# Performance work log

Measured on AMD Instinct MI355X. Metric: run time of the kernel, lower is better.

The kernel has to match this reference:

```python
import jax, jax.numpy as jnp
import numpy as np

EPS = 1e-5
NEG = jnp.float32(-1e30)


def _mha(q_in, kv, in_w, in_b, out_w, out_b, n_heads, allowed=None):
    # torch nn.MultiheadAttention (batch_first, eval mode)
    B, Nq, D = q_in.shape
    hd = D // n_heads
    wq, wk, wv = jnp.split(in_w, 3, axis=0)
    bq, bk, bv = jnp.split(in_b, 3)
    q = (q_in @ wq.T + bq).reshape(B, Nq, n_heads, hd).transpose(0, 2, 1, 3)
    k = (kv @ wk.T + bk).reshape(B, -1, n_heads, hd).transpose(0, 2, 1, 3)
    v = (kv @ wv.T + bv).reshape(B, -1, n_heads, hd).transpose(0, 2, 1, 3)
    s = jnp.einsum('bhqd,bhkd->bhqk', q, k) / jnp.sqrt(jnp.float32(hd))
    if allowed is not None:
        s = jnp.where(allowed[:, None, :, :], s, NEG)
    a = jax.nn.softmax(s, axis=-1)
    o = jnp.einsum('bhqk,bhkd->bhqd', a, v).transpose(0, 2, 1, 3).reshape(B, Nq, D)
    o = o @ out_w.T + out_b
    if allowed is not None:
        # rows with no allowed keys: torch would NaN; we zero them (deterministic)
        o = jnp.where(allowed.any(-1)[..., None], o, 0.0)
    return o


def _layernorm(x, g, b):
    mu = x.mean(-1, keepdims=True)
    var = ((x - mu) ** 2).mean(-1, keepdims=True)
    return (x - mu) * jax.lax.rsqrt(var + EPS) * g + b


def setup_inputs() -> dict:
    key = jax.random.key(0)
    B, N, D, NH = 128, 128, 512, 8
    ks = jax.random.split(key, 16)
    s = 0.02
    return {
        'H': jax.random.normal(ks[0], (B, N, D), jnp.float32),
        'pred_heads': jax.random.randint(ks[1], (B, N), 0, N, jnp.int32),
        'mask': jnp.ones((B, N), jnp.int32),
        'head_in_w': jax.random.normal(ks[2], (3 * D, D)) * s,
        'head_in_b': jnp.zeros((3 * D,), jnp.float32),
        'head_out_w': jax.random.normal(ks[3], (D, D)) * s,
        'head_out_b': jnp.zeros((D,), jnp.float32),
        'sib_in_w': jax.random.normal(ks[4], (3 * D, D)) * s,
        'sib_in_b': jnp.zeros((3 * D,), jnp.float32),
        'sib_out_w': jax.random.normal(ks[5], (D, D)) * s,
        'sib_out_b': jnp.zeros((D,), jnp.float32),
        'child_w': jax.random.normal(ks[6], (D, 2 * D)) * s,
        'child_b': jnp.zeros((D,), jnp.float32),
        'gate_w': jax.random.normal(ks[7], (D, 4 * D)) * s,
        'gate_b': jnp.zeros((D,), jnp.float32),
        'trans_w': jax.random.normal(ks[8], (D, 4 * D)) * s,
        'trans_b': jnp.zeros((D,), jnp.float32),
        'ln_g': jnp.ones((D,), jnp.float32),
        'ln_b': jnp.zeros((D,), jnp.float32),
    }


def reference(H, pred_heads, mask, head_in_w, head_in_b, head_out_w, head_out_b,
              sib_in_w, sib_in_b, sib_out_w, sib_out_b, child_w, child_b,
              gate_w, gate_b, trans_w, trans_b, ln_g, ln_b):
    B, N, D = H.shape
    NH = 8
    heads = jnp.clip(pred_heads, 0, N - 1)  # [B,N]
    maskb = mask.astype(bool)

    # 1) head message: gather each node's head repr, attend Q=H, K=V=head_repr
    head_repr = jnp.take_along_axis(H, heads[..., None], axis=1)  # [B,N,D]
    head_msg = _mha(H, head_repr, head_in_w, head_in_b, head_out_w, head_out_b, NH)

    # 2) child aggregation: vectorized scatter-add replacing the Python loop.
    # loop runs d in [1, length) with mask a prefix -> valid = mask & (d >= 1)
    valid = maskb & (jnp.arange(N) >= 1)  # [B,N]
    contrib = H * valid[..., None].astype(H.dtype)
    flat_idx = (jnp.arange(B)[:, None] * N + heads).reshape(-1)
    child_sum = jnp.zeros((B * N, D), H.dtype).at[flat_idx].add(
        contrib.reshape(B * N, D)).reshape(B, N, D)
    child_count = jnp.zeros((B * N,), H.dtype).at[flat_idx].add(
        valid.reshape(-1).astype(H.dtype)).reshape(B, N, 1)
    child_avg = child_sum / jnp.maximum(child_count, 1.0)
    child_msg = jax.nn.gelu(
        jnp.concatenate([H, child_avg], -1) @ child_w.T + child_b,
        approximate=False)

    # 3) sibling attention (N <= 128 branch): same head, not self, both masked-in
    same_head = heads[:, :, None] == heads[:, None, :]
    eye = jnp.eye(N, dtype=bool)[None]
    allowed = same_head & ~eye & maskb[:, None, :] & maskb[:, :, None]
    sib_msg = _mha(H, H, sib_in_w, sib_in_b, sib_out_w, sib_out_b, NH, allowed=allowed)

    # 4) gated fusion + residual + layernorm
    combined = jnp.concatenate([H, head_msg, child_msg, sib_msg], -1)
    gate = jax.nn.sigmoid(combined @ gate_w.T + gate_b)
    update = jax.nn.gelu(combined @ trans_w.T + trans_b, approximate=False)
    return _layernorm(H + gate * update, ln_g, ln_b)
```

## Files before the change

### kernel.cpp

```cpp
#include <hip/hip_runtime.h>
#include <hip/hip_bf16.h>

typedef __bf16 bf16x8 __attribute__((ext_vector_type(8)));
typedef float f32x4 __attribute__((ext_vector_type(4)));

__device__ __forceinline__ void gload16(const void* g, void* l) {
  __builtin_amdgcn_global_load_lds(
      (const __attribute__((address_space(1))) unsigned int*)g,
      (__attribute__((address_space(3))) unsigned int*)l, 16, 0, 0);
}

__device__ __forceinline__ float gelu_f(float x) {
  return 0.5f * x * (1.f + erff(x * 0.70710678118654752f));
}
__device__ __forceinline__ float sigmoid_f(float x) {
  return 1.f / (1.f + __expf(-x));
}

template<int EPI>
__global__ __launch_bounds__(512, 2)
void gemm8_kernel(const __hip_bfloat16* __restrict__ A0, int lda0,
                  const __hip_bfloat16* __restrict__ A1, int lda1,
                  const __hip_bfloat16* __restrict__ A2, int lda2,
                  int ks1, int ks2,
                  const __hip_bfloat16* __restrict__ B, int ldb,
                  const float* __restrict__ bias,
                  const float* __restrict__ fvec,
                  const float* __restrict__ flags,
                  void* __restrict__ C, int ldc, int K)
{
  extern __shared__ __align__(16) char lds[];
  const int t = threadIdx.x;
  const int l = t & 63;
  const int w = t >> 6;
  const int l15 = l & 15, lg = (l >> 4) & 3;
  const int orig = blockIdx.y * gridDim.x + blockIdx.x;
  const int nwg = gridDim.x * gridDim.y;
  const int gy = gridDim.y;
  const int xcd = orig & 7, rk = orig >> 3, q = nwg >> 3, r = nwg & 7;
  const int bid = (xcd < r ? xcd * (q + 1) : r * (q + 1) + (xcd - r) * q) + rk;
  const int m0 = (bid % gy) * 256;
  const int n0 = (bid / gy) * 256;

  const int srow = t >> 2;
  const int kc8 = ((t & 3) ^ ((t >> 3) & 3)) * 8;
  const int mbase = (w >> 2) * 128;
  const int nbase = (w & 3) * 64;
  const int swz = (l15 >> 1) & 3;
  const int kslot = (lg ^ swz) * 8;
  int aoff[8], boff[4];
#pragma unroll
  for (int mf = 0; mf < 8; ++mf) aoff[mf] = (mbase + mf * 16 + l15) * 32 + kslot;
#pragma unroll
  for (int nf = 0; nf < 4; ++nf) boff[nf] = (nbase + nf * 16 + l15) * 32 + kslot;

  auto segA = [&](int k0, const __hip_bfloat16*& Ap, int& ldA, int& krel) {
    if (k0 >= ks2)      { Ap = A2; ldA = lda2; krel = k0 - ks2; }
    else if (k0 >= ks1) { Ap = A1; ldA = lda1; krel = k0 - ks1; }
    else                { Ap = A0; ldA = lda0; krel = k0; }
  };
  auto stageA = [&](int buf, const __hip_bfloat16* Ap, int ldA, int krel) {
    char* base = lds + buf * 32768 + t * 16;
    gload16(Ap + (size_t)(m0 + srow) * ldA + krel + kc8, base);
    gload16(Ap + (size_t)(m0 + 128 + srow) * ldA + krel + kc8, base + 8192);
  };
  auto stageB = [&](int buf, int k0) {
    char* base = lds + buf * 32768 + 16384 + t * 16;
    gload16(B + (size_t)(n0 + srow) * ldb + k0 + kc8, base);
    gload16(B + (size_t)(n0 + 128 + srow) * ldb + k0 + kc8, base + 8192);
  };

  f32x4 acc[8][4] = {};
  const int NT = K >> 5;

#pragma unroll 1
  for (int pt = 0; pt < 3; ++pt) {
    const __hip_bfloat16* Ap; int ldA, krel;
    segA(pt * 32, Ap, ldA, krel);
    stageA(pt, Ap, ldA, krel);
    stageB(pt, pt * 32);
  }
  asm volatile("s_waitcnt vmcnt(8)" ::: "memory");
  __builtin_amdgcn_s_barrier();
  __builtin_amdgcn_sched_barrier(0);

#pragma unroll 1
  for (int tt = 0; tt < NT; ++tt) {
    const int buf = tt & 3;
    const __hip_bfloat16* As = (const __hip_bfloat16*)(lds + buf * 32768);
    const __hip_bfloat16* Bs = (const __hip_bfloat16*)(lds + buf * 32768 + 16384);
    const int pf = tt + 3;
    const bool do_pf = pf < NT;
    const int pbuf = pf & 3;
    const __hip_bfloat16* Ap = A0; int ldA = lda0, krel = 0;
    if (do_pf) segA(pf * 32, Ap, ldA, krel);

    bf16x8 bv[4], av[4];
#pragma unroll
    for (int nf = 0; nf < 4; ++nf) bv[nf] = *(const bf16x8*)(Bs + boff[nf]);
#pragma unroll
    for (int mf = 0; mf < 4; ++mf) av[mf] = *(const bf16x8*)(As + aoff[mf]);
    if (do_pf) stageA(pbuf, Ap, ldA, krel);
    __builtin_amdgcn_s_setprio(1);
#pragma unroll
    for (int mf = 0; mf < 4; ++mf)
#pragma unroll
      for (int nf = 0; nf < 4; ++nf)
        acc[mf][nf] = __builtin_amdgcn_mfma_f32_16x16x32_bf16(av[mf], bv[nf], acc[mf][nf], 0, 0, 0);
    __builtin_amdgcn_s_setprio(0);

#pragma unroll
    for (int mf = 0; mf < 4; ++mf) av[mf] = *(const bf16x8*)(As + aoff[mf + 4]);
    if (do_pf) stageB(pbuf, pf * 32);
    __builtin_amdgcn_s_setprio(1);
#pragma unroll
    for (int mf = 0; mf < 4; ++mf)
#pragma unroll
      for (int nf = 0; nf < 4; ++nf)
        acc[mf + 4][nf] = __builtin_amdgcn_mfma_f32_16x16x32_bf16(av[mf], bv[nf], acc[mf + 4][nf], 0, 0, 0);
    __builtin_amdgcn_s_setprio(0);

    __builtin_amdgcn_sched_barrier(0);
    if (tt + 3 < NT)      asm volatile("s_waitcnt vmcnt(8)" ::: "memory");
    else if (tt + 2 < NT) asm volatile("s_waitcnt vmcnt(4)" ::: "memory");
    else if (tt + 1 < NT) asm volatile("s_waitcnt vmcnt(0)" ::: "memory");
    if (tt + 1 < NT) {
      __builtin_amdgcn_s_barrier();
      __builtin_amdgcn_sched_barrier(0);
    }
  }

  if (EPI == 2) {
#pragma unroll
    for (int mf = 0; mf < 8; ++mf) {
#pragma unroll
      for (int nh = 0; nh < 2; ++nh) {
        const int nf = nh * 2;
        const int sc = n0 + nbase + nf * 16;
        const float bg = bias[sc + l15], bt = bias[sc + 16 + l15];
        const float fg = fvec[sc + l15], ft = fvec[sc + 16 + l15];
        const int ocol = (sc >> 5) * 16 + l15;
#pragma unroll
        for (int j = 0; j < 4; ++j) {
          const int row = m0 + mbase + mf * 16 + lg * 4 + j;
          const float flg = flags[row];
          float g  = acc[mf][nf][j]     + bg + flg * fg;
          float tv = acc[mf][nf + 1][j] + bt + flg * ft;
          ((__hip_bfloat16*)C)[(size_t)row * ldc + ocol] =
              __float2bfloat16(sigmoid_f(g) * gelu_f(tv));
        }
      }
    }
    return;
  }
#pragma unroll
  for (int mf = 0; mf < 8; ++mf)
#pragma unroll
    for (int nf = 0; nf < 4; ++nf) {
      const int col = n0 + nbase + nf * 16 + l15;
      const float bc = bias ? bias[col] : 0.f;
#pragma unroll
      for (int j = 0; j < 4; ++j) {
        const int row = m0 + mbase + mf * 16 + lg * 4 + j;
        ((__hip_bfloat16*)C)[(size_t)row * ldc + col] =
            __float2bfloat16(acc[mf][nf][j] + bc);
      }
    }
}

template<int EPI, bool OBF16>
__global__ __launch_bounds__(256)
void gemm_kernel(const __hip_bfloat16* __restrict__ A0, int lda0,
                 const __hip_bfloat16* __restrict__ A1, int lda1,
                 const __hip_bfloat16* __restrict__ A2, int lda2,
                 int ks1, int ks2,
                 const __hip_bfloat16* __restrict__ B, int ldb,
                 const float* __restrict__ bias,
                 const float* __restrict__ fvec,
                 const float* __restrict__ flags,
                 void* __restrict__ C, int ldc, int K)
{
  __shared__ __align__(16) __hip_bfloat16 As[128 * 32];
  __shared__ __align__(16) __hip_bfloat16 Bs[128 * 32];
  const int t = threadIdx.x;
  const int l = t & 63, w = t >> 6;
  const int gx = gridDim.x;
  int bid = blockIdx.y * gx + blockIdx.x;
  {
    const int nwg = gx * gridDim.y;
    const int xcd = bid & 7, rk = bid >> 3, q = nwg >> 3, r = nwg & 7;
    bid = (xcd < r ? xcd * (q + 1) : r * (q + 1) + (xcd - r) * q) + rk;
  }
  const int m0 = (bid / gx) * 128, n0 = (bid % gx) * 128;
  const int wm = (w >> 1) * 64, wn = (w & 1) * 64;
  const int l15 = l & 15, lg = l >> 4;

  const int r0 = t >> 2;
  const int kk0 = ((t & 3) ^ ((t >> 3) & 3)) * 8;
  char* lA = (char*)As + t * 16;
  char* lB = (char*)Bs + t * 16;
  const size_t boff1 = (size_t)(n0 + r0) * ldb + kk0;
  const size_t boff2 = (size_t)(n0 + r0 + 64) * ldb + kk0;

  int aoffR[4], boffR[4];
#pragma unroll
  for (int i = 0; i < 4; ++i) {
    const int ra = wm + i * 16 + l15;
    aoffR[i] = ra * 32 + ((lg ^ ((ra >> 1) & 3)) * 8);
    const int rb = wn + i * 16 + l15;
    boffR[i] = rb * 32 + ((lg ^ ((rb >> 1) & 3)) * 8);
  }
  f32x4 acc[4][4] = {};

#pragma unroll 1
  for (int seg = 0; seg < 3; ++seg) {
    const __hip_bfloat16* Ap;
    int ldA, kb, ke;
    if (seg == 0)      { Ap = A0; ldA = lda0; kb = 0;   ke = ks1; }
    else if (seg == 1) { Ap = A1; ldA = lda1; kb = ks1; ke = ks2; }
    else               { Ap = A2; ldA = lda2; kb = ks2; ke = K;   }
    if (kb >= ke) continue;
    const size_t aoff1 = (size_t)(m0 + r0) * ldA + kk0;
    const size_t aoff2 = (size_t)(m0 + r0 + 64) * ldA + kk0;
    for (int k0 = kb; k0 < ke; k0 += 32) {
      const int kr = k0 - kb;
      gload16(Ap + aoff1 + kr, lA);
      gload16(Ap + aoff2 + kr, lA + 4096);
      gload16(B + boff1 + k0, lB);
      gload16(B + boff2 + k0, lB + 4096);
      __syncthreads();
      bf16x8 af[4], bfr[4];
#pragma unroll
      for (int i = 0; i < 4; ++i) {
        af[i]  = *(const bf16x8*)((const __hip_bfloat16*)As + aoffR[i]);
        bfr[i] = *(const bf16x8*)((const __hip_bfloat16*)Bs + boffR[i]);
      }
#pragma unroll
      for (int mi = 0; mi < 4; ++mi)
#pragma unroll
        for (int ni = 0; ni < 4; ++ni)
          acc[mi][ni] = __builtin_amdgcn_mfma_f32_16x16x32_bf16(af[mi], bfr[ni], acc[mi][ni], 0, 0, 0);
      __syncthreads();
    }
  }

#pragma unroll
  for (int mi = 0; mi < 4; ++mi)
#pragma unroll
    for (int ni = 0; ni < 4; ++ni) {
      const int col = n0 + wn + ni * 16 + l15;
      const float bc = bias ? bias[col] : 0.f;
#pragma unroll
      for (int j = 0; j < 4; ++j) {
        const int row = m0 + wm + mi * 16 + lg * 4 + j;
        float v = acc[mi][ni][j] + bc;
        if (EPI == 1) v = gelu_f(v);
        if (OBF16) ((__hip_bfloat16*)C)[(size_t)row * ldc + col] = __float2bfloat16(v);
        else       ((float*)C)[(size_t)row * ldc + col] = v;
      }
    }
}

__global__ __launch_bounds__(256)
void attn_kernel(const __hip_bfloat16* __restrict__ QKV,
                 const int* __restrict__ pred_heads,
                 const int* __restrict__ mask,
                 __hip_bfloat16* __restrict__ Oout,
                 float* __restrict__ flags)
{
  __shared__ __align__(16) __hip_bfloat16 smem[128 * 128];
  __shared__ __align__(16) __hip_bfloat16 Vt[64 * 128];
  __shared__ int hs[128];
  __shared__ int mk[128];
  const bool SIB = blockIdx.x >= 1024;
  const int bh = blockIdx.x & 1023;
  const int b = bh >> 3, h = bh & 7;
  const int qofs = SIB ? 1536 : 0;
  __hip_bfloat16* Ob = Oout + (SIB ? 512 : 0);
  const int t = threadIdx.x, l = t & 63, w = t >> 6;
  const int l15 = l & 15, lg = l >> 4;
  __hip_bfloat16* Qs = smem;
  __hip_bfloat16* Ks = smem + 128 * 64;

  if (t < 128) {
    int hh = pred_heads[b * 128 + t];
    hh = hh < 0 ? 0 : (hh > 127 ? 127 : hh);
    hs[t] = hh;
    mk[t] = mask[b * 128 + t];
  }
  __syncthreads();
  const size_t tb = (size_t)b * 128 * 3072;
  const int co = qofs + h * 64;
#pragma unroll
  for (int it = 0; it < 4; ++it) {
    const int idx = it * 256 + t;
    const int row = idx >> 3;
    const int c8 = (idx & 7) * 8;
    const int sl = ((c8 >> 3) ^ (row & 7)) * 8;
    *(uint4*)(Qs + row * 64 + sl) = *(const uint4*)(QKV + tb + (size_t)row * 3072 + co + c8);
    const int krow = SIB ? row : hs[row];
    *(uint4*)(Ks + row * 64 + sl) = *(const uint4*)(QKV + tb + (size_t)krow * 3072 + co + 512 + c8);
    uint4 vv = *(const uint4*)(QKV + tb + (size_t)krow * 3072 + co + 1024 + c8);
    const __hip_bfloat16* vp = (const __hip_bfloat16*)&vv;
#pragma unroll
    for (int u = 0; u < 8; ++u) {
      const int d = c8 + u;
      Vt[d * 128 + (((row >> 3) ^ (d & 7)) * 8) + (row & 7)] = vp[u];
    }
  }
  __syncthreads();

  const int r0 = w * 32;
  f32x4 s[2][8] = {};
  const int x7 = l15 & 7;
#pragma unroll
  for (int ks = 0; ks < 2; ++ks) {
    const int sl = ((ks * 4 + lg) ^ x7) * 8;
    bf16x8 qa0 = *(const bf16x8*)(Qs + (r0 + l15) * 64 + sl);
    bf16x8 qa1 = *(const bf16x8*)(Qs + (r0 + 16 + l15) * 64 + sl);
#pragma unroll
    for (int nj = 0; nj < 8; ++nj) {
      bf16x8 kb = *(const bf16x8*)(Ks + (nj * 16 + l15) * 64 + sl);
      s[0][nj] = __builtin_amdgcn_mfma_f32_16x16x32_bf16(qa0, kb, s[0][nj], 0, 0, 0);
      s[1][nj] = __builtin_amdgcn_mfma_f32_16x16x32_bf16(qa1, kb, s[1][nj], 0, 0, 0);
    }
  }
  const float scale = 0.125f;
  float inv_sum[2][4];
#pragma unroll
  for (int mi = 0; mi < 2; ++mi) {
#pragma unroll
    for (int j = 0; j < 4; ++j) {
      const int row = r0 + mi * 16 + lg * 4 + j;
      float mx = -1e30f;
#pragma unroll
      for (int nj = 0; nj < 8; ++nj) {
        float v = s[mi][nj][j] * scale;
        bool ok = true;
        if (SIB) {
          int c = nj * 16 + l15;
          ok = (hs[row] == hs[c]) && (row != c) && mk[row] && mk[c];
        }
        mx = fmaxf(mx, ok ? v : -1e30f);
      }
#pragma unroll
      for (int m = 1; m < 16; m <<= 1) mx = fmaxf(mx, __shfl_xor(mx, m));
      float sum = 0.f;
#pragma unroll
      for (int nj = 0; nj < 8; ++nj) {
        float v = s[mi][nj][j] * scale;
        bool ok = true;
        if (SIB) {
          int c = nj * 16 + l15;
          ok = (hs[row] == hs[c]) && (row != c) && mk[row] && mk[c];
        }
        float p = ok ? __expf(v - mx) : 0.f;
        s[mi][nj][j] = p;
        sum += p;
      }
#pragma unroll
      for (int m = 1; m < 16; m <<= 1) sum += __shfl_xor(sum, m);
      inv_sum[mi][j] = sum > 0.f ? 1.f / sum : 0.f;
    }
  }
  __syncthreads();
#pragma unroll
  for (int mi = 0; mi < 2; ++mi)
#pragma unroll
    for (int nj = 0; nj < 8; ++nj)
#pragma unroll
      for (int j = 0; j < 4; ++j) {
        const int rr = r0 + mi * 16 + lg * 4 + j;
        const int cc = nj * 16 + l15;
        smem[rr * 128 + (((cc >> 3) ^ (rr & 7)) * 8) + (cc & 7)] = __float2bfloat16(s[mi][nj][j]);
      }
  __syncthreads();

  f32x4 o[2][4] = {};
#pragma unroll
  for (int js = 0; js < 4; ++js) {
    const int slot = js * 4 + lg;
    const int slp = (slot ^ x7) * 8;
    bf16x8 pa0 = *(const bf16x8*)(smem + (r0 + l15) * 128 + slp);
    bf16x8 pa1 = *(const bf16x8*)(smem + (r0 + 16 + l15) * 128 + slp);
#pragma unroll
    for (int dj = 0; dj < 4; ++dj) {
      bf16x8 vb = *(const bf16x8*)(Vt + (dj * 16 + l15) * 128 + slp);
      o[0][dj] = __builtin_amdgcn_mfma_f32_16x16x32_bf16(pa0, vb, o[0][dj], 0, 0, 0);
      o[1][dj] = __builtin_amdgcn_mfma_f32_16x16x32_bf16(pa1, vb, o[1][dj], 0, 0, 0);
    }
  }
  const int hb = h * 64;
#pragma unroll
  for (int mi = 0; mi < 2; ++mi)
#pragma unroll
    for (int dj = 0; dj < 4; ++dj)
#pragma unroll
      for (int j = 0; j < 4; ++j) {
        const int row = r0 + mi * 16 + lg * 4 + j;
        const int dc = dj * 16 + l15;
        const float val = o[mi][dj][j] * inv_sum[mi][j];
        Ob[(size_t)(b * 128 + row) * 1024 + hb + dc] = __float2bfloat16(val);
      }
  if (SIB && h == 0 && l15 == 0) {
#pragma unroll
    for (int mi = 0; mi < 2; ++mi)
#pragma unroll
      for (int j = 0; j < 4; ++j) {
        const int row = r0 + mi * 16 + lg * 4 + j;
        flags[b * 128 + row] = inv_sum[mi][j] > 0.f ? 1.f : 0.f;
      }
  }
}

__global__ __launch_bounds__(256)
void child_kernel(const __hip_bfloat16* __restrict__ Hbf,
                  const int* __restrict__ pred_heads,
                  const int* __restrict__ mask,
                  __hip_bfloat16* __restrict__ Cavg)
{
  __shared__ float sum[128 * 64];
  __shared__ int cnt[128];
  __shared__ int hsl[128];
  __shared__ int vld[128];
  const int t = threadIdx.x;
  const int b = blockIdx.y, ch = blockIdx.x;
#pragma unroll
  for (int u = 0; u < 32; ++u) sum[u * 256 + t] = 0.f;
  if (t < 128) {
    int hh = pred_heads[b * 128 + t];
    hh = hh < 0 ? 0 : (hh > 127 ? 127 : hh);
    hsl[t] = hh;
    vld[t] = (mask[b * 128 + t] != 0) && (t >= 1);
    cnt[t] = 0;
  }
  __syncthreads();
  if (t < 128 && vld[t]) atomicAdd(&cnt[hsl[t]], 1);
  __syncthreads();
  const int c = t & 63;
  const int isub = t >> 6;
  for (int ii = 0; ii < 32; ++ii) {
    int i = ii * 4 + isub;
    if (vld[i])
      atomicAdd(&sum[hsl[i] * 64 + c],
                __bfloat162float(Hbf[((size_t)b * 128 + i) * 512 + ch * 64 + c]));
  }
  __syncthreads();
#pragma unroll
  for (int u = 0; u < 32; ++u) {
    int idx = u * 256 + t;
    int p = idx >> 6, cc = idx & 63;
    float avg = sum[idx] / fmaxf((float)cnt[p], 1.f);
    Cavg[((size_t)b * 128 + p) * 512 + ch * 64 + cc] = __float2bfloat16(avg);
  }
}

__global__ void prep_kernel(const float* __restrict__ hin_w, const float* __restrict__ sin_w,
                            const float* __restrict__ ch_w, const float* __restrict__ H,
                            __hip_bfloat16* __restrict__ Wqkv, __hip_bfloat16* __restrict__ Wch,
                            __hip_bfloat16* __restrict__ Hbf,
                            const float* __restrict__ gw, const float* __restrict__ tw,
                            const float* __restrict__ gb, const float* __restrict__ tb,
                            __hip_bfloat16* __restrict__ Wf, __hip_bfloat16* __restrict__ Whin,
                            __hip_bfloat16* __restrict__ Wsin, float* __restrict__ bias,
                            const float* __restrict__ hout_w, const float* __restrict__ sout_w,
                            __hip_bfloat16* __restrict__ WhoT, __hip_bfloat16* __restrict__ WsoT)
{
  int gid = blockIdx.x * 256 + threadIdx.x;
  if (gid < 2621440) {
    const float* s; __hip_bfloat16* d; int i;
    if      (gid <  196608) { s = hin_w; d = Wqkv;          i = gid; }
    else if (gid <  393216) { s = sin_w; d = Wqkv + 786432; i = gid - 196608; }
    else if (gid <  524288) { s = ch_w;  d = Wch;           i = gid - 393216; }
    else                    { s = H;     d = Hbf;           i = gid - 524288; }
    i *= 4;
    float4 v = *(const float4*)(s + i);
    union { __hip_bfloat16 h[4]; uint2 u; } p;
    p.h[0] = __float2bfloat16(v.x); p.h[1] = __float2bfloat16(v.y);
    p.h[2] = __float2bfloat16(v.z); p.h[3] = __float2bfloat16(v.w);
    *(uint2*)(d + i) = p.u;
  } else if (gid < 4718592) {
    int idx = gid - 2621440;
    int s = idx >> 11, c = idx & 2047;
    int q = s >> 5, r = s & 31;
    float v = (r < 16) ? gw[(size_t)(q * 16 + r) * 2048 + c]
                       : tw[(size_t)(q * 16 + r - 16) * 2048 + c];
    __hip_bfloat16 hv = __float2bfloat16(v);
    if      (c <  512) Wf[(size_t)s * 2048 + c] = hv;
    else if (c < 1024) Whin[(size_t)s * 512 + (c - 512)] = hv;
    else if (c < 1536) Wf[(size_t)s * 2048 + (c - 512)] = hv;
    else               Wsin[(size_t)s * 512 + (c - 1536)] = hv;
    if (c == 0) bias[s] = (r < 16) ? gb[q * 16 + r] : tb[q * 16 + r - 16];
  } else {
    int idx = gid - 4718592;
    const float* s = hout_w; __hip_bfloat16* d = WhoT;
    if (idx >= 262144) { s = sout_w; d = WsoT; idx -= 262144; }
    int i = idx >> 9, j = idx & 511;
    d[i * 512 + j] = __float2bfloat16(s[(size_t)j * 512 + i]);
  }
}

__global__ __launch_bounds__(256)
void foldbias_kernel(const __hip_bfloat16* __restrict__ Whin, const __hip_bfloat16* __restrict__ Wsin,
                     const float* __restrict__ hob, const float* __restrict__ sob,
                     float* __restrict__ bias_gt, float* __restrict__ fvec)
{
  const int s = blockIdx.x * 256 + threadIdx.x;
  float a = 0.f, c = 0.f;
  for (int j = 0; j < 512; j += 8) {
    bf16x8 wh = *(const bf16x8*)(Whin + (size_t)s * 512 + j);
    bf16x8 wsv = *(const bf16x8*)(Wsin + (size_t)s * 512 + j);
#pragma unroll
    for (int u = 0; u < 8; ++u) {
      a += (float)wh[u] * hob[j + u];
      c += (float)wsv[u] * sob[j + u];
    }
  }
  bias_gt[s] += a;
  fvec[s] = c;
}

__global__ __launch_bounds__(64)
void ln_kernel(const float* __restrict__ H, const __hip_bfloat16* __restrict__ U,
               const float* __restrict__ g, const float* __restrict__ bta,
               float* __restrict__ out)
{
  const int row = blockIdx.x, l = threadIdx.x;
  const size_t hb = (size_t)row * 512;
  const int c0 = l * 8;
  float4 h0 = *(const float4*)(H + hb + c0);
  float4 h1 = *(const float4*)(H + hb + c0 + 4);
  bf16x8 uv = *(const bf16x8*)(U + hb + c0);
  float x[8];
  x[0] = h0.x + (float)uv[0]; x[1] = h0.y + (float)uv[1];
  x[2] = h0.z + (float)uv[2]; x[3] = h0.w + (float)uv[3];
  x[4] = h1.x + (float)uv[4]; x[5] = h1.y + (float)uv[5];
  x[6] = h1.z + (float)uv[6]; x[7] = h1.w + (float)uv[7];
  float sum = 0.f;
#pragma unroll
  for (int u = 0; u < 8; ++u) sum += x[u];
#pragma unroll
  for (int m = 32; m; m >>= 1) sum += __shfl_xor(sum, m);
  const float mean = sum * (1.f / 512.f);
  float vs = 0.f;
#pragma unroll
  for (int u = 0; u < 8; ++u) { float d0 = x[u] - mean; vs += d0 * d0; }
#pragma unroll
  for (int m = 32; m; m >>= 1) vs += __shfl_xor(vs, m);
  const float rstd = rsqrtf(vs * (1.f / 512.f) + 1e-5f);
  float4 g0 = *(const float4*)(g + c0);
  float4 g1 = *(const float4*)(g + c0 + 4);
  float4 b0 = *(const float4*)(bta + c0);
  float4 b1 = *(const float4*)(bta + c0 + 4);
  float4 o0, o1;
  o0.x = (x[0] - mean) * rstd * g0.x + b0.x;
  o0.y = (x[1] - mean) * rstd * g0.y + b0.y;
  o0.z = (x[2] - mean) * rstd * g0.z + b0.z;
  o0.w = (x[3] - mean) * rstd * g0.w + b0.w;
  o1.x = (x[4] - mean) * rstd * g1.x + b1.x;
  o1.y = (x[5] - mean) * rstd * g1.y + b1.y;
  o1.z = (x[6] - mean) * rstd * g1.z + b1.z;
  o1.w = (x[7] - mean) * rstd * g1.w + b1.w;
  *(float4*)(out + hb + c0) = o0;
  *(float4*)(out + hb + c0 + 4) = o1;
}

extern "C" void kernel_launch(void* const* d_in, const int* in_sizes, int n_in,
                              void* d_out, int out_size, void* d_ws, size_t ws_size,
                              hipStream_t stream)
{
  (void)in_sizes; (void)n_in; (void)out_size; (void)ws_size;
  const float* H      = (const float*)d_in[0];
  const int*  pred    = (const int*)d_in[1];
  const int*  maskp   = (const int*)d_in[2];
  const float* hin_w  = (const float*)d_in[3];
  const float* hin_b  = (const float*)d_in[4];
  const float* hout_w = (const float*)d_in[5];
  const float* hout_b = (const float*)d_in[6];
  const float* sin_w  = (const float*)d_in[7];
  const float* sin_b  = (const float*)d_in[8];
  const float* sout_w = (const float*)d_in[9];
  const float* sout_b = (const float*)d_in[10];
  const float* ch_w   = (const float*)d_in[11];
  const float* ch_b   = (const float*)d_in[12];
  const float* g_w    = (const float*)d_in[13];
  const float* g_b    = (const float*)d_in[14];
  const float* t_w    = (const float*)d_in[15];
  const float* t_b    = (const float*)d_in[16];
  const float* lng    = (const float*)d_in[17];
  const float* lnb    = (const float*)d_in[18];

  char* ws = (char*)d_ws;
  __hip_bfloat16* Wqkv  = (__hip_bfloat16*)(ws + 0);
  __hip_bfloat16* Wch   = (__hip_bfloat16*)(ws + 3145728);
  __hip_bfloat16* Wgt   = (__hip_bfloat16*)(ws + 4194304);
  float* bias_qkv       = (float*)(ws + 8388608);
  float* bias_gt        = (float*)(ws + 8400896);
  float* fvec           = (float*)(ws + 8404992);
  float* flags          = (float*)(ws + 8409088);
  __hip_bfloat16* Hbf   = (__hip_bfloat16*)(ws + 8474624);
  char* QKVr            = ws + 25251840;
  __hip_bfloat16* QKV   = (__hip_bfloat16*)QKVr;
  __hip_bfloat16* Whin  = (__hip_bfloat16*)(QKVr + 0);
  __hip_bfloat16* Wsin  = (__hip_bfloat16*)(QKVr + 1048576);
  __hip_bfloat16* WhoT  = (__hip_bfloat16*)(QKVr + 2097152);
  __hip_bfloat16* WsoT  = (__hip_bfloat16*)(QKVr + 2621440);
  __hip_bfloat16* CHM   = (__hip_bfloat16*)(QKVr + 0);
  __hip_bfloat16* U     = (__hip_bfloat16*)(QKVr + 16777216);
  __hip_bfloat16* Cavg  = (__hip_bfloat16*)(QKVr + 50331648);
  __hip_bfloat16* CM2   = (__hip_bfloat16*)(ws + 125915136);

  hipFuncSetAttribute(reinterpret_cast<const void*>(gemm8_kernel<0>),
                      hipFuncAttributeMaxDynamicSharedMemorySize, 131072);
  hipFuncSetAttribute(reinterpret_cast<const void*>(gemm8_kernel<2>),
                      hipFuncAttributeMaxDynamicSharedMemorySize, 131072);

  prep_kernel<<<20480, 256, 0, stream>>>(hin_w, sin_w, ch_w, H, Wqkv, Wch, Hbf,
                                         g_w, t_w, g_b, t_b, Wgt, Whin, Wsin, bias_gt,
                                         hout_w, sout_w, WhoT, WsoT);
  foldbias_kernel<<<4, 256, 0, stream>>>(Whin, Wsin, hout_b, sout_b, bias_gt, fvec);
  hipMemcpyAsync(bias_qkv, hin_b, 1536 * 4, hipMemcpyDeviceToDevice, stream);
  hipMemcpyAsync(bias_qkv + 1536, sin_b, 1536 * 4, hipMemcpyDeviceToDevice, stream);

  gemm_kernel<0, true><<<dim3(4, 8), 256, 0, stream>>>(
      Whin, 512, Whin, 512, Whin, 512, 512, 512, WhoT, 512,
      (const float*)nullptr, (const float*)nullptr, (const float*)nullptr,
      (void*)(Wgt + 1024), 2048, 512);
  gemm_kernel<0, true><<<dim3(4, 8), 256, 0, stream>>>(
      Wsin, 512, Wsin, 512, Wsin, 512, 512, 512, WsoT, 512,
      (const float*)nullptr, (const float*)nullptr, (const float*)nullptr,
      (void*)(Wgt + 1536), 2048, 512);

  gemm8_kernel<0><<<dim3(12, 64), 512, 131072, stream>>>(
      Hbf, 512, Hbf, 512, Hbf, 512, 512, 512, Wqkv, 512,
      bias_qkv, (const float*)nullptr, (const float*)nullptr,
      (void*)QKV, 3072, 512);

  attn_kernel<<<2048, 256, 0, stream>>>(QKV, pred, maskp, CM2, flags);

  child_kernel<<<dim3(8, 128), 256, 0, stream>>>(Hbf, pred, maskp, Cavg);
  gemm_kernel<1, true><<<dim3(4, 128), 256, 0, stream>>>(
      Hbf, 512, Cavg, 512, Cavg, 512, 512, 1024, Wch, 1024,
      ch_b, (const float*)nullptr, (const float*)nullptr,
      (void*)CHM, 512, 1024);

  gemm8_kernel<2><<<dim3(4, 64), 512, 131072, stream>>>(
      Hbf, 512, CHM, 512, CM2, 1024, 512, 1024, Wgt, 2048,
      bias_gt, fvec, flags, (void*)U, 512, 2048);

  ln_kernel<<<16384, 64, 0, stream>>>(H, U, lng, lnb, (float*)d_out);
}
```

Baseline: 509.0 us.

## Transpose QK^T MFMA to get per-lane query rows and bitmask sibling masking

Swaps the MFMA operands so each lane holds one query row across key columns. The row max and sum then need only two cross-lane shuffles instead of four. The sibling mask is precomputed as a per-row 32-bit bitmask from one combined key array that folds the mask into the head index. Probabilities are normalized before the bf16 store, written to LDS as packed 8-byte chunks, and the final output scaling is dropped. Normalizing before bf16 rounding slightly changes numerics.

After: 453.9 us. -10.8%, faster.

```diff
diff --git a/kernel.cpp b/kernel.cpp
--- a/kernel.cpp
+++ b/kernel.cpp
@@ -271,7 +271,7 @@
   __shared__ __align__(16) __hip_bfloat16 smem[128 * 128];
   __shared__ __align__(16) __hip_bfloat16 Vt[64 * 128];
   __shared__ int hs[128];
-  __shared__ int mk[128];
+  __shared__ int key[128];
   const bool SIB = blockIdx.x >= 1024;
   const int bh = blockIdx.x & 1023;
   const int b = bh >> 3, h = bh & 7;
@@ -286,7 +286,7 @@
     int hh = pred_heads[b * 128 + t];
     hh = hh < 0 ? 0 : (hh > 127 ? 127 : hh);
     hs[t] = hh;
-    mk[t] = mask[b * 128 + t];
+    key[t] = mask[b * 128 + t] ? hh : (128 + t);
   }
   __syncthreads();
   const size_t tb = (size_t)b * 128 * 3072;
@@ -311,76 +311,96 @@
   __syncthreads();
 
   const int r0 = w * 32;
-  f32x4 s[2][8] = {};
   const int x7 = l15 & 7;
+  f32x4 s[8][2] = {};
 #pragma unroll
   for (int ks = 0; ks < 2; ++ks) {
     const int sl = ((ks * 4 + lg) ^ x7) * 8;
-    bf16x8 qa0 = *(const bf16x8*)(Qs + (r0 + l15) * 64 + sl);
-    bf16x8 qa1 = *(const bf16x8*)(Qs + (r0 + 16 + l15) * 64 + sl);
-#pragma unroll
-    for (int nj = 0; nj < 8; ++nj) {
-      bf16x8 kb = *(const bf16x8*)(Ks + (nj * 16 + l15) * 64 + sl);
-      s[0][nj] = __builtin_amdgcn_mfma_f32_16x16x32_bf16(qa0, kb, s[0][nj], 0, 0, 0);
-      s[1][nj] = __builtin_amdgcn_mfma_f32_16x16x32_bf16(qa1, kb, s[1][nj], 0, 0, 0);
-    }
-  }
+    bf16x8 qb0 = *(const bf16x8*)(Qs + (r0 + l15) * 64 + sl);
+    bf16x8 qb1 = *(const bf16x8*)(Qs + (r0 + 16 + l15) * 64 + sl);
+#pragma unroll
+    for (int kf = 0; kf < 8; ++kf) {
+      bf16x8 ka = *(const bf16x8*)(Ks + (kf * 16 + l15) * 64 + sl);
+      s[kf][0] = __builtin_amdgcn_mfma_f32_16x16x32_bf16(ka, qb0, s[kf][0], 0, 0, 0);
+      s[kf][1] = __builtin_amdgcn_mfma_f32_16x16x32_bf16(ka, qb1, s[kf][1], 0, 0, 0);
+    }
+  }
+
   const float scale = 0.125f;
-  float inv_sum[2][4];
-#pragma unroll
-  for (int mi = 0; mi < 2; ++mi) {
-#pragma unroll
-    for (int j = 0; j < 4; ++j) {
-      const int row = r0 + mi * 16 + lg * 4 + j;
-      float mx = -1e30f;
-#pragma unroll
-      for (int nj = 0; nj < 8; ++nj) {
-        float v = s[mi][nj][j] * scale;
-        bool ok = true;
-        if (SIB) {
-          int c = nj * 16 + l15;
-          ok = (hs[row] == hs[c]) && (row != c) && mk[row] && mk[c];
+  int kq[2] = {0, 0};
+  int4 kv[8];
+  if (SIB) {
+    kq[0] = key[r0 + l15];
+    kq[1] = key[r0 + 16 + l15];
+#pragma unroll
+    for (int kf = 0; kf < 8; ++kf) kv[kf] = *(const int4*)&key[kf * 16 + lg * 4];
+  }
+  float invs[2];
+#pragma unroll
+  for (int qf = 0; qf < 2; ++qf) {
+    const int q = r0 + qf * 16 + l15;
+    unsigned om = 0xFFFFFFFFu;
+    if (SIB) {
+      om = 0u;
+#pragma unroll
+      for (int kf = 0; kf < 8; ++kf) {
+        const int* kp = (const int*)&kv[kf];
+#pragma unroll
+        for (int j = 0; j < 4; ++j) {
+          const int k = kf * 16 + lg * 4 + j;
+          if (kp[j] == kq[qf] && k != q) om |= (1u << (kf * 4 + j));
         }
-        mx = fmaxf(mx, ok ? v : -1e30f);
-      }
-#pragma unroll
-      for (int m = 1; m < 16; m <<= 1) mx = fmaxf(mx, __shfl_xor(mx, m));
-      float sum = 0.f;
-#pragma unroll
-      for (int nj = 0; nj < 8; ++nj) {
-        float v = s[mi][nj][j] * scale;
-        bool ok = true;
-        if (SIB) {
-          int c = nj * 16 + l15;
-          ok = (hs[row] == hs[c]) && (row != c) && mk[row] && mk[c];
-        }
-        float p = ok ? __expf(v - mx) : 0.f;
-        s[mi][nj][j] = p;
+      }
+    }
+    float mx = -1e30f;
+#pragma unroll
+    for (int kf = 0; kf < 8; ++kf)
+#pragma unroll
+      for (int j = 0; j < 4; ++j) {
+        const float v = s[kf][qf][j] * scale;
+        mx = fmaxf(mx, ((om >> (kf * 4 + j)) & 1u) ? v : -1e30f);
+      }
+    mx = fmaxf(mx, __shfl_xor(mx, 16));
+    mx = fmaxf(mx, __shfl_xor(mx, 32));
+    float sum = 0.f;
+#pragma unroll
+    for (int kf = 0; kf < 8; ++kf)
+#pragma unroll
+      for (int j = 0; j < 4; ++j) {
+        const float v = s[kf][qf][j] * scale;
+        const float p = ((om >> (kf * 4 + j)) & 1u) ? __expf(v - mx) : 0.f;
+        s[kf][qf][j] = p;
         sum += p;
       }
-#pragma unroll
-      for (int m = 1; m < 16; m <<= 1) sum += __shfl_xor(sum, m);
-      inv_sum[mi][j] = sum > 0.f ? 1.f / sum : 0.f;
-    }
-  }
+    sum += __shfl_xor(sum, 16);
+    sum += __shfl_xor(sum, 32);
+    invs[qf] = sum > 0.f ? 1.f / sum : 0.f;
+  }
+  if (SIB && h == 0 && lg == 0) {
+    flags[b * 128 + r0 + l15]      = invs[0] > 0.f ? 1.f : 0.f;
+    flags[b * 128 + r0 + 16 + l15] = invs[1] > 0.f ? 1.f : 0.f;
+  }
+
   __syncthreads();
 #pragma unroll
-  for (int mi = 0; mi < 2; ++mi)
-#pragma unroll
-    for (int nj = 0; nj < 8; ++nj)
-#pragma unroll
-      for (int j = 0; j < 4; ++j) {
-        const int rr = r0 + mi * 16 + lg * 4 + j;
-        const int cc = nj * 16 + l15;
-        smem[rr * 128 + (((cc >> 3) ^ (rr & 7)) * 8) + (cc & 7)] = __float2bfloat16(s[mi][nj][j]);
-      }
+  for (int qf = 0; qf < 2; ++qf) {
+    const int q = r0 + qf * 16 + l15;
+    const int base = q * 128 + ((lg & 1) << 2);
+#pragma unroll
+    for (int kf = 0; kf < 8; ++kf) {
+      const int c16 = kf * 2 + (lg >> 1);
+      __hip_bfloat16 pk[4];
+#pragma unroll
+      for (int j = 0; j < 4; ++j) pk[j] = __float2bfloat16(s[kf][qf][j] * invs[qf]);
+      *(uint2*)(smem + base + ((c16 ^ x7) << 3)) = *(const uint2*)pk;
+    }
+  }
   __syncthreads();
 
   f32x4 o[2][4] = {};
 #pragma unroll
   for (int js = 0; js < 4; ++js) {
-    const int slot = js * 4 + lg;
-    const int slp = (slot ^ x7) * 8;
+    const int slp = ((js * 4 + lg) ^ x7) * 8;
     bf16x8 pa0 = *(const bf16x8*)(smem + (r0 + l15) * 128 + slp);
     bf16x8 pa1 = *(const bf16x8*)(smem + (r0 + 16 + l15) * 128 + slp);
 #pragma unroll
@@ -399,18 +419,8 @@
       for (int j = 0; j < 4; ++j) {
         const int row = r0 + mi * 16 + lg * 4 + j;
         const int dc = dj * 16 + l15;
-        const float val = o[mi][dj][j] * inv_sum[mi][j];
-        Ob[(size_t)(b * 128 + row) * 1024 + hb + dc] = __float2bfloat16(val);
-      }
-  if (SIB && h == 0 && l15 == 0) {
-#pragma unroll
-    for (int mi = 0; mi < 2; ++mi)
-#pragma unroll
-      for (int j = 0; j < 4; ++j) {
-        const int row = r0 + mi * 16 + lg * 4 + j;
-        flags[b * 128 + row] = inv_sum[mi][j] > 0.f ? 1.f : 0.f;
-      }
-  }
+        Ob[(size_t)(b * 128 + row) * 1024 + hb + dc] = __float2bfloat16(o[mi][dj][j]);
+      }
 }
 
 __global__ __launch_bounds__(256)
```
